# Kernel optimization log

Measured on AMD Instinct MI355X. Metric: run time of the kernel, lower is better.

## Reference

```python
import jax, jax.numpy as jnp
import numpy as np

D_MODEL = 2048
N_ROOMS = 128
B = 128
S = 512


def setup_inputs() -> dict:
    key = jax.random.key(0)
    ks = jax.random.split(key, 8)
    scale = 1.0 / np.sqrt(D_MODEL)
    x = jax.random.normal(ks[0], (B, S, D_MODEL), dtype=jnp.float32)
    room_summaries = jax.random.normal(ks[1], (N_ROOMS, D_MODEL), dtype=jnp.float32)
    Wc = jax.random.uniform(ks[2], (D_MODEL, D_MODEL), minval=-scale, maxval=scale, dtype=jnp.float32)
    bc = jax.random.uniform(ks[3], (D_MODEL,), minval=-scale, maxval=scale, dtype=jnp.float32)
    Ww = jax.random.uniform(ks[4], (N_ROOMS * N_ROOMS, D_MODEL), minval=-scale, maxval=scale, dtype=jnp.float32)
    bw = jax.random.uniform(ks[5], (N_ROOMS * N_ROOMS,), minval=-scale, maxval=scale, dtype=jnp.float32)
    adjacency = jnp.eye(N_ROOMS, dtype=jnp.float32) + jax.random.normal(ks[6], (N_ROOMS, N_ROOMS), dtype=jnp.float32) * 0.1
    return {"x": x, "room_summaries": room_summaries, "Wc": Wc, "bc": bc,
            "Ww": Ww, "bw": bw, "adjacency": adjacency}


def reference(x, room_summaries, Wc, bc, Ww, bw, adjacency):
    n_rooms = room_summaries.shape[0]
    # context: mean over seq then linear -> [B, d_model]
    context = jnp.mean(x, axis=1) @ Wc.T + bc
    # dynamic warp of adjacency -> [B, N, N]
    warp = (context @ Ww.T + bw).reshape(-1, n_rooms, n_rooms) * 0.1
    adj = jax.nn.softmax(adjacency[None, :, :] + warp, axis=-1)
    # raw room scores: [B, N]
    raw_scores = context @ room_summaries.T
    # adjacency-warped scores: [B, N]
    warped_scores = jnp.einsum('bij,bj->bi', adj, raw_scores)
    return jax.nn.sigmoid(warped_scores)
```

## Files before the change

### kernel.cpp

```cpp
#include <hip/hip_runtime.h>
#include <stdint.h>

#define D_MODEL 2048
#define N_ROOMS 128
#define BATCH   128
#define SEQ     512
#define NN      (N_ROOMS * N_ROOMS)
#define NCOL    (NN + N_ROOMS)

typedef short bf16x8 __attribute__((ext_vector_type(8)));
typedef float f32x4  __attribute__((ext_vector_type(4)));

__device__ __forceinline__ unsigned short f2bf(float f) {
    union { float f; uint32_t u; } c; c.f = f;
    uint32_t u = c.u;
    uint32_t r = (u + 0x7fffu + ((u >> 16) & 1u)) >> 16;
    return (unsigned short)r;
}

__global__ void k_mean_partial(const float* __restrict__ x, float* __restrict__ part) {
    int bx = blockIdx.x;
    int b = bx >> 4, rem = bx & 15;
    int sc = rem >> 1, dc = rem & 1;
    int d = dc * 1024 + threadIdx.x * 4;
    const float* p = x + ((size_t)(b * SEQ + sc * 64)) * D_MODEL + d;
    float ax = 0.f, ay = 0.f, az = 0.f, aw = 0.f;
    #pragma unroll 8
    for (int s = 0; s < 64; ++s) {
        float4 v = *(const float4*)p;
        ax += v.x; ay += v.y; az += v.z; aw += v.w;
        p += D_MODEL;
    }
    float4 o = {ax, ay, az, aw};
    *(float4*)(part + ((size_t)(sc * BATCH + b)) * D_MODEL + d) = o;
}

__global__ void k_mean_combine(const float* __restrict__ part,
                               unsigned short* __restrict__ meanb) {
    int i = (blockIdx.x * 256 + threadIdx.x) * 4;
    float4 s = {0.f, 0.f, 0.f, 0.f};
    #pragma unroll
    for (int sc = 0; sc < 8; ++sc) {
        float4 v = *(const float4*)(part + (size_t)sc * BATCH * D_MODEL + i);
        s.x += v.x; s.y += v.y; s.z += v.z; s.w += v.w;
    }
    const float inv = 1.0f / (float)SEQ;
    ushort4 hv = {f2bf(s.x * inv), f2bf(s.y * inv), f2bf(s.z * inv), f2bf(s.w * inv)};
    *(ushort4*)(meanb + i) = hv;
}

__launch_bounds__(256)
__global__ void k_ctx_gemm(const unsigned short* __restrict__ meanb,
                           const float* __restrict__ Wc,
                           float* __restrict__ ctx_part) {
    __shared__ short A[128 * 72];
    __shared__ short Bt[64 * 72];
    int bx = blockIdx.x;
    int nt = bx & 31, ks = bx >> 5;
    int n0 = nt * 64;
    int k0 = ks * 256;
    int tid = threadIdx.x, lane = tid & 63, w = tid >> 6;
    int mbase = w * 32;
    f32x4 acc[2][4] = {};
    for (int kt = 0; kt < 4; ++kt) {
        int kb = k0 + kt * 64;
        __syncthreads();
        #pragma unroll
        for (int i = 0; i < 4; ++i) {
            int u = tid + 256 * i;
            int row = u >> 3, c = u & 7;
            *(int4*)&A[row * 72 + c * 8] = *(const int4*)(meanb + (size_t)row * D_MODEL + kb + c * 8);
        }
        #pragma unroll
        for (int i = 0; i < 4; ++i) {
            int u = tid + 256 * i;
            int row = u >> 4, c = u & 15;
            float4 v = *(const float4*)(Wc + (size_t)(n0 + row) * D_MODEL + kb + c * 4);
            ushort4 hv = {f2bf(v.x), f2bf(v.y), f2bf(v.z), f2bf(v.w)};
            *(ushort4*)&Bt[row * 72 + c * 4] = hv;
        }
        __syncthreads();
        #pragma unroll
        for (int kk = 0; kk < 64; kk += 32) {
            int ko = kk + (lane >> 4) * 8;
            int mr = mbase + (lane & 15);
            bf16x8 a0 = *(const bf16x8*)&A[mr * 72 + ko];
            bf16x8 a1 = *(const bf16x8*)&A[(mr + 16) * 72 + ko];
            #pragma unroll
            for (int ni = 0; ni < 4; ++ni) {
                bf16x8 bfr = *(const bf16x8*)&Bt[(ni * 16 + (lane & 15)) * 72 + ko];
                acc[0][ni] = __builtin_amdgcn_mfma_f32_16x16x32_bf16(a0, bfr, acc[0][ni], 0, 0, 0);
                acc[1][ni] = __builtin_amdgcn_mfma_f32_16x16x32_bf16(a1, bfr, acc[1][ni], 0, 0, 0);
            }
        }
    }
    int col = lane & 15, quad = lane >> 4;
    #pragma unroll
    for (int mi = 0; mi < 2; ++mi)
        #pragma unroll
        for (int ni = 0; ni < 4; ++ni)
            #pragma unroll
            for (int r = 0; r < 4; ++r) {
                int m = mbase + mi * 16 + quad * 4 + r;
                int n = n0 + ni * 16 + col;
                ctx_part[((size_t)(ks * BATCH + m)) * D_MODEL + n] = acc[mi][ni][r];
            }
}

__global__ void k_ctx_finalize(const float* __restrict__ ctx_part, const float* __restrict__ bc,
                               unsigned short* __restrict__ ctxb) {
    int i = (blockIdx.x * 256 + threadIdx.x) * 4;
    float4 s = {0.f, 0.f, 0.f, 0.f};
    #pragma unroll
    for (int ks = 0; ks < 8; ++ks) {
        float4 v = *(const float4*)(ctx_part + (size_t)ks * BATCH * D_MODEL + i);
        s.x += v.x; s.y += v.y; s.z += v.z; s.w += v.w;
    }
    int d = i & (D_MODEL - 1);
    float4 bias = *(const float4*)(bc + d);
    ushort4 hv = {f2bf(s.x + bias.x), f2bf(s.y + bias.y), f2bf(s.z + bias.z), f2bf(s.w + bias.w)};
    *(ushort4*)(ctxb + i) = hv;
}

__launch_bounds__(256)
__global__ void k_warp_gemm(const unsigned short* __restrict__ ctxb,
                            const float* __restrict__ Ww,
                            const float* __restrict__ room,
                            float* __restrict__ wp) {
    __shared__ short A[128 * 72];
    __shared__ short Bt[64 * 72];
    int bx = blockIdx.x;
    int nt = bx % 258, ks = bx / 258;
    int n0 = nt * 64;
    int k0 = ks * 1024;
    const float* Bsrc = (nt < 256) ? (Ww + (size_t)n0 * D_MODEL)
                                   : (room + (size_t)(n0 - NN) * D_MODEL);
    int tid = threadIdx.x, lane = tid & 63, w = tid >> 6;
    int mbase = w * 32;
    f32x4 acc[2][4] = {};
    for (int kt = 0; kt < 16; ++kt) {
        int kb = k0 + kt * 64;
        __syncthreads();
        #pragma unroll
        for (int i = 0; i < 4; ++i) {
            int u = tid + 256 * i;
            int row = u >> 3, c = u & 7;
            *(int4*)&A[row * 72 + c * 8] = *(const int4*)(ctxb + (size_t)row * D_MODEL + kb + c * 8);
        }
        #pragma unroll
        for (int i = 0; i < 4; ++i) {
            int u = tid + 256 * i;
            int row = u >> 4, c = u & 15;
            float4 v = *(const float4*)(Bsrc + (size_t)row * D_MODEL + kb + c * 4);
            ushort4 hv = {f2bf(v.x), f2bf(v.y), f2bf(v.z), f2bf(v.w)};
            *(ushort4*)&Bt[row * 72 + c * 4] = hv;
        }
        __syncthreads();
        #pragma unroll
        for (int kk = 0; kk < 64; kk += 32) {
            int ko = kk + (lane >> 4) * 8;
            int mr = mbase + (lane & 15);
            bf16x8 a0 = *(const bf16x8*)&A[mr * 72 + ko];
            bf16x8 a1 = *(const bf16x8*)&A[(mr + 16) * 72 + ko];
            #pragma unroll
            for (int ni = 0; ni < 4; ++ni) {
                bf16x8 bfr = *(const bf16x8*)&Bt[(ni * 16 + (lane & 15)) * 72 + ko];
                acc[0][ni] = __builtin_amdgcn_mfma_f32_16x16x32_bf16(a0, bfr, acc[0][ni], 0, 0, 0);
                acc[1][ni] = __builtin_amdgcn_mfma_f32_16x16x32_bf16(a1, bfr, acc[1][ni], 0, 0, 0);
            }
        }
    }
    int col = lane & 15, quad = lane >> 4;
    #pragma unroll
    for (int mi = 0; mi < 2; ++mi)
        #pragma unroll
        for (int ni = 0; ni < 4; ++ni)
            #pragma unroll
            for (int r = 0; r < 4; ++r) {
                int m = mbase + mi * 16 + quad * 4 + r;
                int n = n0 + ni * 16 + col;
                wp[((size_t)(ks * BATCH + m)) * NCOL + n] = acc[mi][ni][r];
            }
}

__global__ void k_epilogue(const float* __restrict__ wp, const float* __restrict__ bw,
                           const float* __restrict__ adj, float* __restrict__ out) {
    int tid = threadIdx.x, lane = tid & 63, w = tid >> 6;
    int row = blockIdx.x * 4 + w;
    int b = row >> 7, i = row & 127;
    int j0 = lane, j1 = lane + 64;
    size_t b0 = (size_t)b * NCOL;
    size_t b1 = (size_t)(BATCH + b) * NCOL;
    int off = i * 128;
    float w0 = wp[b0 + off + j0] + wp[b1 + off + j0];
    float w1 = wp[b0 + off + j1] + wp[b1 + off + j1];
    float r0 = wp[b0 + NN + j0] + wp[b1 + NN + j0];
    float r1 = wp[b0 + NN + j1] + wp[b1 + NN + j1];
    float l0 = adj[off + j0] + 0.1f * (w0 + bw[off + j0]);
    float l1 = adj[off + j1] + 0.1f * (w1 + bw[off + j1]);
    float m = fmaxf(l0, l1);
    #pragma unroll
    for (int o = 32; o; o >>= 1) m = fmaxf(m, __shfl_xor(m, o));
    float p0 = __expf(l0 - m), p1 = __expf(l1 - m);
    float s = p0 + p1;
    float t = p0 * r0 + p1 * r1;
    #pragma unroll
    for (int o = 32; o; o >>= 1) { s += __shfl_xor(s, o); t += __shfl_xor(t, o); }
    if (lane == 0) out[row] = 1.0f / (1.0f + __expf(-(t / s)));
}

extern "C" void kernel_launch(void* const* d_in, const int* in_sizes, int n_in,
                              void* d_out, int out_size, void* d_ws, size_t ws_size,
                              hipStream_t stream) {
    (void)in_sizes; (void)n_in; (void)out_size; (void)ws_size;
    const float* x    = (const float*)d_in[0];
    const float* room = (const float*)d_in[1];
    const float* Wc   = (const float*)d_in[2];
    const float* bc   = (const float*)d_in[3];
    const float* Ww   = (const float*)d_in[4];
    const float* bw   = (const float*)d_in[5];
    const float* adj  = (const float*)d_in[6];
    float* out = (float*)d_out;
    char* ws = (char*)d_ws;
    const size_t MB = 1u << 20;
    float*          part     = (float*)(ws + 0);
    unsigned short* meanb    = (unsigned short*)(ws + 8 * MB);
    float*          ctx_part = (float*)(ws + 9 * MB);
    unsigned short* ctxb     = (unsigned short*)(ws + 17 * MB);
    float*          wp       = (float*)(ws + 18 * MB);

    hipLaunchKernelGGL(k_mean_partial, dim3(2048), dim3(256), 0, stream, x, part);
    hipLaunchKernelGGL(k_mean_combine, dim3(256), dim3(256), 0, stream, part, meanb);
    hipLaunchKernelGGL(k_ctx_gemm, dim3(256), dim3(256), 0, stream, meanb, Wc, ctx_part);
    hipLaunchKernelGGL(k_ctx_finalize, dim3(256), dim3(256), 0, stream, ctx_part, bc, ctxb);
    hipLaunchKernelGGL(k_warp_gemm, dim3(516), dim3(256), 0, stream, ctxb, Ww, room, wp);
    hipLaunchKernelGGL(k_epilogue, dim3(4096), dim3(256), 0, stream, wp, bw, adj, out);
}
```

Baseline: 841.1 us.

## Fuse all stages into one cooperative persistent kernel with grid syncs

Replaces the six separate launches with a single cooperative kernel that runs each stage as a grid-stride loop, separated by grid-wide barriers. This removes per-launch overhead and the gaps between kernels. It also splits the K dimension of the large warp GEMM into four parts so there are more work units, and the epilogue then sums those parts. In exchange, grid syncs add cost, the grid is capped by occupancy, and there is a fallback path to the old multi-kernel launch.

```diff
diff --git a/kernel.cpp b/kernel.cpp
--- a/kernel.cpp
+++ b/kernel.cpp
@@ -1,5 +1,8 @@
 #include <hip/hip_runtime.h>
+#include <hip/hip_cooperative_groups.h>
 #include <stdint.h>
+
+namespace cg = cooperative_groups;
 
 #define D_MODEL 2048
 #define N_ROOMS 128
@@ -7,6 +10,7 @@
 #define SEQ     512
 #define NN      (N_ROOMS * N_ROOMS)
 #define NCOL    (NN + N_ROOMS)
+#define KSW     4
 
 typedef short bf16x8 __attribute__((ext_vector_type(8)));
 typedef float f32x4  __attribute__((ext_vector_type(4)));
@@ -16,6 +20,209 @@
     uint32_t u = c.u;
     uint32_t r = (u + 0x7fffu + ((u >> 16) & 1u)) >> 16;
     return (unsigned short)r;
+}
+
+__launch_bounds__(256, 4)
+__global__ void k_fused(const float* __restrict__ x,
+                        const float* __restrict__ room,
+                        const float* __restrict__ Wc,
+                        const float* __restrict__ bc,
+                        const float* __restrict__ Ww,
+                        const float* __restrict__ bw,
+                        const float* __restrict__ adj,
+                        float* __restrict__ out,
+                        float* __restrict__ part,
+                        unsigned short* __restrict__ meanb,
+                        float* __restrict__ ctx_part,
+                        unsigned short* __restrict__ ctxb,
+                        float* __restrict__ wp) {
+    cg::grid_group gg = cg::this_grid();
+    __shared__ short A[128 * 72];
+    __shared__ short Bt[64 * 72];
+    const int tid = threadIdx.x, lane = tid & 63, w = tid >> 6;
+    const int nb = gridDim.x, bid = blockIdx.x;
+
+    for (int u = bid; u < BATCH * 8; u += nb) {
+        int b = u >> 3, sc = u & 7;
+        const float* p = x + ((size_t)(b * SEQ + sc * 64)) * D_MODEL;
+        float ax = 0.f, ay = 0.f, az = 0.f, aw = 0.f;
+        float cx = 0.f, cy = 0.f, cz = 0.f, cw = 0.f;
+        #pragma unroll 4
+        for (int s = 0; s < 64; ++s) {
+            float4 v0 = *(const float4*)(p + (size_t)s * D_MODEL + tid * 4);
+            float4 v1 = *(const float4*)(p + (size_t)s * D_MODEL + 1024 + tid * 4);
+            ax += v0.x; ay += v0.y; az += v0.z; aw += v0.w;
+            cx += v1.x; cy += v1.y; cz += v1.z; cw += v1.w;
+        }
+        float* q = part + ((size_t)(sc * BATCH + b)) * D_MODEL;
+        float4 o0 = {ax, ay, az, aw};
+        float4 o1 = {cx, cy, cz, cw};
+        *(float4*)(q + tid * 4) = o0;
+        *(float4*)(q + 1024 + tid * 4) = o1;
+    }
+    gg.sync();
+
+    for (int u = bid; u < 256; u += nb) {
+        int i = (u * 256 + tid) * 4;
+        float4 s = {0.f, 0.f, 0.f, 0.f};
+        #pragma unroll
+        for (int sc = 0; sc < 8; ++sc) {
+            float4 v = *(const float4*)(part + (size_t)sc * BATCH * D_MODEL + i);
+            s.x += v.x; s.y += v.y; s.z += v.z; s.w += v.w;
+        }
+        const float inv = 1.0f / (float)SEQ;
+        ushort4 hv = {f2bf(s.x * inv), f2bf(s.y * inv), f2bf(s.z * inv), f2bf(s.w * inv)};
+        *(ushort4*)(meanb + i) = hv;
+    }
+    gg.sync();
+
+    for (int u = bid; u < 256; u += nb) {
+        int nt = u & 31, ks = u >> 5;
+        int n0 = nt * 64, k0 = ks * 256;
+        int mbase = w * 32;
+        f32x4 acc[2][4] = {};
+        for (int kt = 0; kt < 4; ++kt) {
+            int kb = k0 + kt * 64;
+            __syncthreads();
+            #pragma unroll
+            for (int i = 0; i < 4; ++i) {
+                int uu = tid + 256 * i;
+                int row = uu >> 3, c = uu & 7;
+                *(int4*)&A[row * 72 + c * 8] =
+                    *(const int4*)(meanb + (size_t)row * D_MODEL + kb + c * 8);
+            }
+            #pragma unroll
+            for (int i = 0; i < 4; ++i) {
+                int uu = tid + 256 * i;
+                int row = uu >> 4, c = uu & 15;
+                float4 v = *(const float4*)(Wc + (size_t)(n0 + row) * D_MODEL + kb + c * 4);
+                ushort4 hv = {f2bf(v.x), f2bf(v.y), f2bf(v.z), f2bf(v.w)};
+                *(ushort4*)&Bt[row * 72 + c * 4] = hv;
+            }
+            __syncthreads();
+            #pragma unroll
+            for (int kk = 0; kk < 64; kk += 32) {
+                int ko = kk + (lane >> 4) * 8;
+                int mr = mbase + (lane & 15);
+                bf16x8 a0 = *(const bf16x8*)&A[mr * 72 + ko];
+                bf16x8 a1 = *(const bf16x8*)&A[(mr + 16) * 72 + ko];
+                #pragma unroll
+                for (int ni = 0; ni < 4; ++ni) {
+                    bf16x8 bfr = *(const bf16x8*)&Bt[(ni * 16 + (lane & 15)) * 72 + ko];
+                    acc[0][ni] = __builtin_amdgcn_mfma_f32_16x16x32_bf16(a0, bfr, acc[0][ni], 0, 0, 0);
+                    acc[1][ni] = __builtin_amdgcn_mfma_f32_16x16x32_bf16(a1, bfr, acc[1][ni], 0, 0, 0);
+                }
+            }
+        }
+        int col = lane & 15, quad = lane >> 4;
+        #pragma unroll
+        for (int mi = 0; mi < 2; ++mi)
+            #pragma unroll
+            for (int ni = 0; ni < 4; ++ni)
+                #pragma unroll
+                for (int r = 0; r < 4; ++r) {
+                    int m = mbase + mi * 16 + quad * 4 + r;
+                    int n = n0 + ni * 16 + col;
+                    ctx_part[((size_t)(ks * BATCH + m)) * D_MODEL + n] = acc[mi][ni][r];
+                }
+    }
+    gg.sync();
+
+    for (int u = bid; u < 256; u += nb) {
+        int i = (u * 256 + tid) * 4;
+        float4 s = {0.f, 0.f, 0.f, 0.f};
+        #pragma unroll
+        for (int ks = 0; ks < 8; ++ks) {
+            float4 v = *(const float4*)(ctx_part + (size_t)ks * BATCH * D_MODEL + i);
+            s.x += v.x; s.y += v.y; s.z += v.z; s.w += v.w;
+        }
+        int d = i & (D_MODEL - 1);
+        float4 bias = *(const float4*)(bc + d);
+        ushort4 hv = {f2bf(s.x + bias.x), f2bf(s.y + bias.y),
+                      f2bf(s.z + bias.z), f2bf(s.w + bias.w)};
+        *(ushort4*)(ctxb + i) = hv;
+    }
+    gg.sync();
+
+    for (int u = bid; u < 258 * KSW; u += nb) {
+        int nt = u % 258, ks = u / 258;
+        int n0 = nt * 64;
+        int k0 = ks * (D_MODEL / KSW);
+        const float* Bsrc = (nt < 256) ? (Ww + (size_t)n0 * D_MODEL)
+                                       : (room + (size_t)(n0 - NN) * D_MODEL);
+        int mbase = w * 32;
+        f32x4 acc[2][4] = {};
+        for (int kt = 0; kt < (D_MODEL / KSW) / 64; ++kt) {
+            int kb = k0 + kt * 64;
+            __syncthreads();
+            #pragma unroll
+            for (int i = 0; i < 4; ++i) {
+                int uu = tid + 256 * i;
+                int row = uu >> 3, c = uu & 7;
+                *(int4*)&A[row * 72 + c * 8] =
+                    *(const int4*)(ctxb + (size_t)row * D_MODEL + kb + c * 8);
+            }
+            #pragma unroll
+            for (int i = 0; i < 4; ++i) {
+                int uu = tid + 256 * i;
+                int row = uu >> 4, c = uu & 15;
+                float4 v = *(const float4*)(Bsrc + (size_t)row * D_MODEL + kb + c * 4);
+                ushort4 hv = {f2bf(v.x), f2bf(v.y), f2bf(v.z), f2bf(v.w)};
+                *(ushort4*)&Bt[row * 72 + c * 4] = hv;
+            }
+            __syncthreads();
+            #pragma unroll
+            for (int kk = 0; kk < 64; kk += 32) {
+                int ko = kk + (lane >> 4) * 8;
+                int mr = mbase + (lane & 15);
+                bf16x8 a0 = *(const bf16x8*)&A[mr * 72 + ko];
+                bf16x8 a1 = *(const bf16x8*)&A[(mr + 16) * 72 + ko];
+                #pragma unroll
+                for (int ni = 0; ni < 4; ++ni) {
+                    bf16x8 bfr = *(const bf16x8*)&Bt[(ni * 16 + (lane & 15)) * 72 + ko];
+                    acc[0][ni] = __builtin_amdgcn_mfma_f32_16x16x32_bf16(a0, bfr, acc[0][ni], 0, 0, 0);
+                    acc[1][ni] = __builtin_amdgcn_mfma_f32_16x16x32_bf16(a1, bfr, acc[1][ni], 0, 0, 0);
+                }
+            }
+        }
+        int col = lane & 15, quad = lane >> 4;
+        #pragma unroll
+        for (int mi = 0; mi < 2; ++mi)
+            #pragma unroll
+            for (int ni = 0; ni < 4; ++ni)
+                #pragma unroll
+                for (int r = 0; r < 4; ++r) {
+                    int m = mbase + mi * 16 + quad * 4 + r;
+                    int n = n0 + ni * 16 + col;
+                    wp[((size_t)(ks * BATCH + m)) * NCOL + n] = acc[mi][ni][r];
+                }
+    }
+    gg.sync();
+
+    for (int u = bid; u < 4096; u += nb) {
+        int row = u * 4 + w;
+        int b = row >> 7, i = row & 127;
+        int j0 = lane, j1 = lane + 64;
+        int off = i * 128;
+        float w0 = 0.f, w1 = 0.f, r0 = 0.f, r1 = 0.f;
+        #pragma unroll
+        for (int ks = 0; ks < KSW; ++ks) {
+            const float* base = wp + (size_t)(ks * BATCH + b) * NCOL;
+            w0 += base[off + j0]; w1 += base[off + j1];
+            r0 += base[NN + j0];  r1 += base[NN + j1];
+        }
+        float l0 = adj[off + j0] + 0.1f * (w0 + bw[off + j0]);
+        float l1 = adj[off + j1] + 0.1f * (w1 + bw[off + j1]);
+        float m = fmaxf(l0, l1);
+        #pragma unroll
+        for (int o = 32; o; o >>= 1) m = fmaxf(m, __shfl_xor(m, o));
+        float p0 = __expf(l0 - m), p1 = __expf(l1 - m);
+        float s = p0 + p1;
+        float t = p0 * r0 + p1 * r1;
+        #pragma unroll
+        for (int o = 32; o; o >>= 1) { s += __shfl_xor(s, o); t += __shfl_xor(t, o); }
+        if (lane == 0) out[row] = 1.0f / (1.0f + __expf(-(t / s)));
+    }
 }
 
 __global__ void k_mean_partial(const float* __restrict__ x, float* __restrict__ part) {
@@ -229,10 +436,41 @@
     unsigned short* ctxb     = (unsigned short*)(ws + 17 * MB);
     float*          wp       = (float*)(ws + 18 * MB);
 
-    hipLaunchKernelGGL(k_mean_partial, dim3(2048), dim3(256), 0, stream, x, part);
-    hipLaunchKernelGGL(k_mean_combine, dim3(256), dim3(256), 0, stream, part, meanb);
-    hipLaunchKernelGGL(k_ctx_gemm, dim3(256), dim3(256), 0, stream, meanb, Wc, ctx_part);
-    hipLaunchKernelGGL(k_ctx_finalize, dim3(256), dim3(256), 0, stream, ctx_part, bc, ctxb);
-    hipLaunchKernelGGL(k_warp_gemm, dim3(516), dim3(256), 0, stream, ctxb, Ww, room, wp);
-    hipLaunchKernelGGL(k_epilogue, dim3(4096), dim3(256), 0, stream, wp, bw, adj, out);
-}
+    static int coop_grid = -1;
+    if (coop_grid < 0) {
+        int nbpc = 0;
+        if (hipOccupancyMaxActiveBlocksPerMultiprocessor(
+                &nbpc, (const void*)k_fused, 256, 0) != hipSuccess || nbpc < 1) {
+            coop_grid = 0;
+        } else {
+            int g = nbpc * 256;
+            coop_grid = (g < 1024) ? g : 1024;
+        }
+    }
+
+    bool launched = false;
+    if (coop_grid > 0) {
+        void* args[] = {
+            (void*)&x, (void*)&room, (void*)&Wc, (void*)&bc, (void*)&Ww,
+            (void*)&bw, (void*)&adj, (void*)&out,
+            (void*)&part, (void*)&meanb, (void*)&ctx_part, (void*)&ctxb, (void*)&wp
+        };
+        hipError_t err = hipLaunchCooperativeKernel((const void*)k_fused,
+                                                    dim3(coop_grid), dim3(256),
+                                                    args, 0, stream);
+        if (err == hipSuccess) {
+            launched = true;
+        } else {
+            coop_grid = 0;
+        }
+    }
+
+    if (!launched) {
+        hipLaunchKernelGGL(k_mean_partial, dim3(2048), dim3(256), 0, stream, x, part);
+        hipLaunchKernelGGL(k_mean_combine, dim3(256), dim3(256), 0, stream, part, meanb);
+        hipLaunchKernelGGL(k_ctx_gemm, dim3(256), dim3(256), 0, stream, meanb, Wc, ctx_part);
+        hipLaunchKernelGGL(k_ctx_finalize, dim3(256), dim3(256), 0, stream, ctx_part, bc, ctxb);
+        hipLaunchKernelGGL(k_warp_gemm, dim3(516), dim3(256), 0, stream, ctxb, Ww, room, wp);
+        hipLaunchKernelGGL(k_epilogue, dim3(4096), dim3(256), 0, stream, wp, bw, adj, out);
+    }
+}
```

New measurement: 1.092 ms. 29.8% more time.

## Fuse warp GEMM with softmax epilogue into one per-room kernel

Applied to the files above, without the earlier changes.

Replaces the split-K warp GEMM plus separate epilogue kernel with one kernel. Each block owns one room row i and half the batch, computes the 128 warp logits and the room scores, and does the softmax-weighted reduction in shared memory, writing the sigmoid output directly. This removes the large intermediate buffer write and reread and one kernel launch. In exchange the room-summary matrix is recomputed by every block (128 times redundantly), the grid drops to 256 blocks of 512 threads, and split-K is removed, so each block loops over the full K dimension.

```diff
diff --git a/kernel.cpp b/kernel.cpp
--- a/kernel.cpp
+++ b/kernel.cpp
@@ -6,7 +6,6 @@
 #define BATCH   128
 #define SEQ     512
 #define NN      (N_ROOMS * N_ROOMS)
-#define NCOL    (NN + N_ROOMS)
 
 typedef short bf16x8 __attribute__((ext_vector_type(8)));
 typedef float f32x4  __attribute__((ext_vector_type(4)));
@@ -122,36 +121,41 @@
     *(ushort4*)(ctxb + i) = hv;
 }
 
-__launch_bounds__(256)
-__global__ void k_warp_gemm(const unsigned short* __restrict__ ctxb,
-                            const float* __restrict__ Ww,
-                            const float* __restrict__ room,
-                            float* __restrict__ wp) {
-    __shared__ short A[128 * 72];
-    __shared__ short Bt[64 * 72];
-    int bx = blockIdx.x;
-    int nt = bx % 258, ks = bx / 258;
-    int n0 = nt * 64;
-    int k0 = ks * 1024;
-    const float* Bsrc = (nt < 256) ? (Ww + (size_t)n0 * D_MODEL)
-                                   : (room + (size_t)(n0 - NN) * D_MODEL);
-    int tid = threadIdx.x, lane = tid & 63, w = tid >> 6;
-    int mbase = w * 32;
-    f32x4 acc[2][4] = {};
-    for (int kt = 0; kt < 16; ++kt) {
-        int kb = k0 + kt * 64;
-        __syncthreads();
-        #pragma unroll
-        for (int i = 0; i < 4; ++i) {
-            int u = tid + 256 * i;
-            int row = u >> 3, c = u & 7;
-            *(int4*)&A[row * 72 + c * 8] = *(const int4*)(ctxb + (size_t)row * D_MODEL + kb + c * 8);
-        }
-        #pragma unroll
-        for (int i = 0; i < 4; ++i) {
-            int u = tid + 256 * i;
+__launch_bounds__(512)
+__global__ void k_wepi(const unsigned short* __restrict__ ctxb,
+                       const float* __restrict__ Ww,
+                       const float* __restrict__ room,
+                       const float* __restrict__ bw,
+                       const float* __restrict__ adj,
+                       float* __restrict__ out) {
+    __shared__ short A[64 * 72];
+    __shared__ short Bt[256 * 72];
+    __shared__ float red[3][4][64];
+    const int i_room = blockIdx.x & 127;
+    const int half   = blockIdx.x >> 7;
+    const int tid = threadIdx.x, lane = tid & 63, w = tid >> 6;
+    const int wm = w & 1, wn = w >> 1;
+    const int mbase = wm * 32, jbase = wn * 32;
+    const size_t wwbase = (size_t)i_room * 128 * D_MODEL;
+
+    f32x4 aw[2][2] = {};
+    f32x4 ar[2][2] = {};
+
+    for (int kt = 0; kt < 32; ++kt) {
+        int kb = kt * 64;
+        __syncthreads();
+        {
+            int row = tid >> 3, c = tid & 7;
+            *(int4*)&A[row * 72 + c * 8] =
+                *(const int4*)(ctxb + (size_t)(half * 64 + row) * D_MODEL + kb + c * 8);
+        }
+        #pragma unroll
+        for (int it = 0; it < 8; ++it) {
+            int u = tid + 512 * it;
             int row = u >> 4, c = u & 15;
-            float4 v = *(const float4*)(Bsrc + (size_t)row * D_MODEL + kb + c * 4);
+            const float* src = (row < 128) ? (Ww + wwbase + (size_t)row * D_MODEL)
+                                           : (room + (size_t)(row - 128) * D_MODEL);
+            float4 v = *(const float4*)(src + kb + c * 4);
             ushort4 hv = {f2bf(v.x), f2bf(v.y), f2bf(v.z), f2bf(v.w)};
             *(ushort4*)&Bt[row * 72 + c * 4] = hv;
         }
@@ -163,50 +167,65 @@
             bf16x8 a0 = *(const bf16x8*)&A[mr * 72 + ko];
             bf16x8 a1 = *(const bf16x8*)&A[(mr + 16) * 72 + ko];
             #pragma unroll
-            for (int ni = 0; ni < 4; ++ni) {
-                bf16x8 bfr = *(const bf16x8*)&Bt[(ni * 16 + (lane & 15)) * 72 + ko];
-                acc[0][ni] = __builtin_amdgcn_mfma_f32_16x16x32_bf16(a0, bfr, acc[0][ni], 0, 0, 0);
-                acc[1][ni] = __builtin_amdgcn_mfma_f32_16x16x32_bf16(a1, bfr, acc[1][ni], 0, 0, 0);
-            }
-        }
-    }
-    int col = lane & 15, quad = lane >> 4;
+            for (int ni = 0; ni < 2; ++ni) {
+                int br = jbase + ni * 16 + (lane & 15);
+                bf16x8 bW = *(const bf16x8*)&Bt[br * 72 + ko];
+                bf16x8 bR = *(const bf16x8*)&Bt[(128 + br) * 72 + ko];
+                aw[0][ni] = __builtin_amdgcn_mfma_f32_16x16x32_bf16(a0, bW, aw[0][ni], 0, 0, 0);
+                aw[1][ni] = __builtin_amdgcn_mfma_f32_16x16x32_bf16(a1, bW, aw[1][ni], 0, 0, 0);
+                ar[0][ni] = __builtin_amdgcn_mfma_f32_16x16x32_bf16(a0, bR, ar[0][ni], 0, 0, 0);
+                ar[1][ni] = __builtin_amdgcn_mfma_f32_16x16x32_bf16(a1, bR, ar[1][ni], 0, 0, 0);
+            }
+        }
+    }
+
+    const int col = lane & 15, quad = lane >> 4;
+    float adj0 = adj[i_room * 128 + jbase + col];
+    float adj1 = adj[i_room * 128 + jbase + 16 + col];
+    float bw0  = bw[i_room * 128 + jbase + col];
+    float bw1  = bw[i_room * 128 + jbase + 16 + col];
+
+    float l0[2][4], l1[2][4];
     #pragma unroll
     for (int mi = 0; mi < 2; ++mi)
         #pragma unroll
-        for (int ni = 0; ni < 4; ++ni)
+        for (int r = 0; r < 4; ++r) {
+            l0[mi][r] = adj0 + 0.1f * (aw[mi][0][r] + bw0);
+            l1[mi][r] = adj1 + 0.1f * (aw[mi][1][r] + bw1);
+            float m2 = fmaxf(l0[mi][r], l1[mi][r]);
+            #pragma unroll
+            for (int o = 1; o < 16; o <<= 1) m2 = fmaxf(m2, __shfl_xor(m2, o));
+            if (col == 0) red[0][wn][mbase + mi * 16 + quad * 4 + r] = m2;
+        }
+    __syncthreads();
+    #pragma unroll
+    for (int mi = 0; mi < 2; ++mi)
+        #pragma unroll
+        for (int r = 0; r < 4; ++r) {
+            int rl = mbase + mi * 16 + quad * 4 + r;
+            float m = fmaxf(fmaxf(red[0][0][rl], red[0][1][rl]),
+                            fmaxf(red[0][2][rl], red[0][3][rl]));
+            float p0 = __expf(l0[mi][r] - m);
+            float p1 = __expf(l1[mi][r] - m);
+            float s = p0 + p1;
+            float t = p0 * ar[mi][0][r] + p1 * ar[mi][1][r];
+            #pragma unroll
+            for (int o = 1; o < 16; o <<= 1) { s += __shfl_xor(s, o); t += __shfl_xor(t, o); }
+            if (col == 0) { red[1][wn][rl] = s; red[2][wn][rl] = t; }
+        }
+    __syncthreads();
+    if (wn == 0 && col == 0) {
+        #pragma unroll
+        for (int mi = 0; mi < 2; ++mi)
             #pragma unroll
             for (int r = 0; r < 4; ++r) {
-                int m = mbase + mi * 16 + quad * 4 + r;
-                int n = n0 + ni * 16 + col;
-                wp[((size_t)(ks * BATCH + m)) * NCOL + n] = acc[mi][ni][r];
-            }
-}
-
-__global__ void k_epilogue(const float* __restrict__ wp, const float* __restrict__ bw,
-                           const float* __restrict__ adj, float* __restrict__ out) {
-    int tid = threadIdx.x, lane = tid & 63, w = tid >> 6;
-    int row = blockIdx.x * 4 + w;
-    int b = row >> 7, i = row & 127;
-    int j0 = lane, j1 = lane + 64;
-    size_t b0 = (size_t)b * NCOL;
-    size_t b1 = (size_t)(BATCH + b) * NCOL;
-    int off = i * 128;
-    float w0 = wp[b0 + off + j0] + wp[b1 + off + j0];
-    float w1 = wp[b0 + off + j1] + wp[b1 + off + j1];
-    float r0 = wp[b0 + NN + j0] + wp[b1 + NN + j0];
-    float r1 = wp[b0 + NN + j1] + wp[b1 + NN + j1];
-    float l0 = adj[off + j0] + 0.1f * (w0 + bw[off + j0]);
-    float l1 = adj[off + j1] + 0.1f * (w1 + bw[off + j1]);
-    float m = fmaxf(l0, l1);
-    #pragma unroll
-    for (int o = 32; o; o >>= 1) m = fmaxf(m, __shfl_xor(m, o));
-    float p0 = __expf(l0 - m), p1 = __expf(l1 - m);
-    float s = p0 + p1;
-    float t = p0 * r0 + p1 * r1;
-    #pragma unroll
-    for (int o = 32; o; o >>= 1) { s += __shfl_xor(s, o); t += __shfl_xor(t, o); }
-    if (lane == 0) out[row] = 1.0f / (1.0f + __expf(-(t / s)));
+                int rl = mbase + mi * 16 + quad * 4 + r;
+                float s = red[1][0][rl] + red[1][1][rl] + red[1][2][rl] + red[1][3][rl];
+                float t = red[2][0][rl] + red[2][1][rl] + red[2][2][rl] + red[2][3][rl];
+                out[(size_t)(half * 64 + rl) * N_ROOMS + i_room] =
+                    1.0f / (1.0f + __expf(-(t / s)));
+            }
+    }
 }
 
 extern "C" void kernel_launch(void* const* d_in, const int* in_sizes, int n_in,
@@ -227,12 +246,10 @@
     unsigned short* meanb    = (unsigned short*)(ws + 8 * MB);
     float*          ctx_part = (float*)(ws + 9 * MB);
     unsigned short* ctxb     = (unsigned short*)(ws + 17 * MB);
-    float*          wp       = (float*)(ws + 18 * MB);
 
     hipLaunchKernelGGL(k_mean_partial, dim3(2048), dim3(256), 0, stream, x, part);
     hipLaunchKernelGGL(k_mean_combine, dim3(256), dim3(256), 0, stream, part, meanb);
     hipLaunchKernelGGL(k_ctx_gemm, dim3(256), dim3(256), 0, stream, meanb, Wc, ctx_part);
     hipLaunchKernelGGL(k_ctx_finalize, dim3(256), dim3(256), 0, stream, ctx_part, bc, ctxb);
-    hipLaunchKernelGGL(k_warp_gemm, dim3(516), dim3(256), 0, stream, ctxb, Ww, room, wp);
-    hipLaunchKernelGGL(k_epilogue, dim3(4096), dim3(256), 0, stream, wp, bw, adj, out);
-}
+    hipLaunchKernelGGL(k_wepi, dim3(256), dim3(512), 0, stream, ctxb, Ww, room, bw, adj, out);
+}
```

After: 909.4 us. 8.1% more time.
